# Kernel tuning notes

Measured on AMD Instinct MI355X. Metric: run time of the kernel, lower is better.

The kernel has to match this reference:

```python
import jax, jax.numpy as jnp
import numpy as np

N_HEADS = 4
ITERS = 3
EPS = 1e-8


def layer_norm(x, g, b, eps=1e-5):
    m = jnp.mean(x, axis=-1, keepdims=True)
    v = jnp.mean((x - m) ** 2, axis=-1, keepdims=True)
    return (x - m) * jax.lax.rsqrt(v + eps) * g + b


def gru_cell(x, h, Wih, Whh, bih, bhh):
    # PyTorch GRUCell semantics. x: [M, kvq], h: [M, dim]
    gi = x @ Wih.T + bih
    gh = h @ Whh.T + bhh
    ir, iz, i_n = jnp.split(gi, 3, axis=-1)
    hr, hz, h_n = jnp.split(gh, 3, axis=-1)
    r = jax.nn.sigmoid(ir + hr)
    z = jax.nn.sigmoid(iz + hz)
    n = jnp.tanh(i_n + r * h_n)
    return (1.0 - z) * n + z * h


def slot_attention(features, slots, Wq, Wk, Wv, g_in, b_in, g_s, b_s, Wih, Whh, bih, bhh):
    b, n, _ = features.shape
    _, ns, dim = slots.shape
    kvq = Wk.shape[0]
    dh = kvq // N_HEADS
    scale = dh ** -0.5
    inp = layer_norm(features, g_in, b_in)
    k = (inp @ Wk.T).reshape(b, n, N_HEADS, dh)
    v = (inp @ Wv.T).reshape(b, n, N_HEADS, dh)
    attn_vis = None
    for _ in range(ITERS):
        slots_prev = slots
        s = layer_norm(slots, g_s, b_s)
        q = (s @ Wq.T).reshape(b, ns, N_HEADS, dh)
        dots = jnp.einsum("bihd,bjhd->bihj", q, k) * scale
        attn = jax.nn.softmax(dots, axis=1)  # competitive softmax over slots
        attn_vis = attn.mean(axis=2)  # [b, ns, n]
        w = attn + EPS
        w = w / jnp.sum(w, axis=-1, keepdims=True)  # weighted mean over features
        upd = jnp.einsum("bjhd,bihj->bihd", v, w).reshape(b, ns, kvq)
        slots = gru_cell(upd.reshape(-1, kvq), slots_prev.reshape(-1, dim),
                         Wih, Whh, bih, bhh).reshape(b, ns, dim)
    return slots, attn_vis


def vq_pool(x, codebook):
    # x: [b, ns, d], codebook: [C, d]
    d2 = (jnp.sum(x ** 2, axis=-1, keepdims=True)
          - 2.0 * jnp.einsum("bnd,cd->bnc", x, codebook)
          + jnp.sum(codebook ** 2, axis=-1))
    idx = jnp.argmin(d2, axis=-1)
    q = codebook[idx]
    commit = jnp.mean((x - jax.lax.stop_gradient(q)) ** 2)
    q = x + jax.lax.stop_gradient(q - x)  # straight-through
    return q, idx, commit


def setup_inputs() -> dict:
    key = jax.random.key(0)
    ks = jax.random.split(key, 16)
    B, N, FD = 32, 1024, 768
    NS, D, KVQ, C = 24, 256, 256, 512
    sc = lambda d: d ** -0.5
    return {
        "features": jax.random.normal(ks[0], (B, N, FD), jnp.float32),
        "conditioning": jax.random.normal(ks[1], (B, NS, D), jnp.float32),
        "Wq": jax.random.normal(ks[2], (KVQ, D), jnp.float32) * sc(D),
        "Wk": jax.random.normal(ks[3], (KVQ, FD), jnp.float32) * sc(FD),
        "Wv": jax.random.normal(ks[4], (KVQ, FD), jnp.float32) * sc(FD),
        "g_in": jnp.ones((FD,), jnp.float32),
        "b_in": jnp.zeros((FD,), jnp.float32),
        "g_s": jnp.ones((D,), jnp.float32),
        "b_s": jnp.zeros((D,), jnp.float32),
        "Wih": jax.random.normal(ks[5], (3 * D, KVQ), jnp.float32) * sc(KVQ),
        "Whh": jax.random.normal(ks[6], (3 * D, D), jnp.float32) * sc(D),
        "bih": jnp.zeros((3 * D,), jnp.float32),
        "bhh": jnp.zeros((3 * D,), jnp.float32),
        "codebook": jax.random.normal(ks[7], (C, D), jnp.float32) * sc(D),
    }


def reference(features, conditioning, Wq, Wk, Wv, g_in, b_in, g_s, b_s,
              Wih, Whh, bih, bhh, codebook):
    sa = lambda f, s: slot_attention(f, s, Wq, Wk, Wv, g_in, b_in, g_s, b_s,
                                     Wih, Whh, bih, bhh)
    slots, pre_attn = sa(features, conditioning)
    q_slots, indices, commit = vq_pool(slots, codebook)
    slots, post_attn = sa(features, q_slots)
    return slots, post_attn, pre_attn, indices, commit
```

## Files before the change

### kernel.cpp

```cpp
#include <hip/hip_runtime.h>
#include <math.h>

#define LB __launch_bounds__(256)

constexpr int BATCH = 32, NFEAT = 1024, FDIM = 768, NSLOT = 24;
constexpr int NH = 4, DH = 64, NITER = 3;
constexpr int MF = BATCH * NFEAT;
constexpr int MS = BATCH * NSLOT;
constexpr float QSCALE = 0.125f;
constexpr float ATTN_EPS = 1e-8f;
constexpr float LNEPS = 1e-5f;

typedef __attribute__((ext_vector_type(8))) short bf16x8;
typedef __attribute__((ext_vector_type(4))) float f32x4;

__device__ __forceinline__ unsigned short f2bf(float x) {
  unsigned u = __float_as_uint(x);
  return (unsigned short)((u + 0x7FFFu + ((u >> 16) & 1u)) >> 16);
}
__device__ __forceinline__ float bf2f(unsigned short h) {
  return __uint_as_float(((unsigned)h) << 16);
}
__device__ __forceinline__ void cvt8(const float4& a, const float4& b, float m, float r,
                                     int4& hi, int4& lo) {
  float v[8] = {a.x, a.y, a.z, a.w, b.x, b.y, b.z, b.w};
  unsigned sh[8], sl[8];
#pragma unroll
  for (int j = 0; j < 8; ++j) {
    float vv = (v[j] - m) * r;
    unsigned short h = f2bf(vv);
    sh[j] = h;
    sl[j] = f2bf(vv - bf2f(h));
  }
  hi = make_int4((int)(sh[0] | (sh[1] << 16)), (int)(sh[2] | (sh[3] << 16)),
                 (int)(sh[4] | (sh[5] << 16)), (int)(sh[6] | (sh[7] << 16)));
  lo = make_int4((int)(sl[0] | (sl[1] << 16)), (int)(sl[2] | (sl[3] << 16)),
                 (int)(sl[4] | (sl[5] << 16)), (int)(sl[6] | (sl[7] << 16)));
}

__device__ __forceinline__ void gll16(const void* g, void* l) {
  __builtin_amdgcn_global_load_lds(
      (const __attribute__((address_space(1))) void*)g,
      (__attribute__((address_space(3))) void*)l, 16, 0, 0);
}

__global__ LB void k_preprow(const float* __restrict__ x, float* __restrict__ stats,
                             const float* __restrict__ Wk, const float* __restrict__ Wv,
                             const float* __restrict__ Wq,
                             const float* __restrict__ g_in, const float* __restrict__ b_in,
                             const float* __restrict__ g_s, const float* __restrict__ b_s,
                             short* __restrict__ Bh_g, short* __restrict__ Bl_g,
                             short* __restrict__ Wgqh, short* __restrict__ Wgql,
                             float* __restrict__ cconst) {
  const int t = threadIdx.x;
  if (blockIdx.x < MF / 4) {
    const int row = blockIdx.x * 4 + (t >> 6);
    const int lane = t & 63;
    const float* xr = x + (size_t)row * FDIM;
    float s = 0.f, sq = 0.f;
#pragma unroll
    for (int i = 0; i < 3; ++i) {
      float4 v = *(const float4*)(xr + i * 256 + lane * 4);
      s += v.x + v.y + v.z + v.w;
      sq += v.x * v.x + v.y * v.y + v.z * v.z + v.w * v.w;
    }
#pragma unroll
    for (int o = 32; o > 0; o >>= 1) { s += __shfl_down(s, o, 64); sq += __shfl_down(sq, o, 64); }
    if (lane == 0) {
      float m = s / (float)FDIM;
      float var = sq / (float)FDIM - m * m;
      stats[row * 2] = m;
      stats[row * 2 + 1] = 1.f / sqrtf(var + LNEPS);
    }
    return;
  }
  const int r = blockIdx.x - MF / 4;
  float s = 0.f;
  if (r < 512) {
    const float* srcW = (r < 256) ? (Wk + (size_t)r * FDIM) : (Wv + (size_t)(r - 256) * FDIM);
    for (int k = t; k < FDIM; k += 256) {
      float w = srcW[k];
      float wg = w * g_in[k];
      s += b_in[k] * w;
      unsigned short h = f2bf(wg);
      Bh_g[(size_t)r * FDIM + k] = (short)h;
      Bl_g[(size_t)r * FDIM + k] = (short)f2bf(wg - bf2f(h));
    }
  } else {
    const int c = r - 512;
    float w = Wq[(size_t)c * 256 + t];
    float wg = w * g_s[t];
    unsigned short hh = f2bf(wg);
    Wgqh[(size_t)c * 256 + t] = (short)hh;
    Wgql[(size_t)c * 256 + t] = (short)f2bf(wg - bf2f(hh));
    s = b_s[t] * w;
  }
  __shared__ float red[256];
  red[t] = s; __syncthreads();
  for (int o = 128; o > 0; o >>= 1) { if (t < o) red[t] += red[t + o]; __syncthreads(); }
  if (t == 0) cconst[r] = red[0];
}

union SmemM {
  struct { short Ah[2048], Al[2048], Bh[2][4096], Bl[2][4096]; } m;
  struct { short vh[128][72], vl[128][72]; } e;
};

__global__ LB void k_mfkv(const float* __restrict__ x, const float* __restrict__ stats,
                          const short* __restrict__ Bh_g, const short* __restrict__ Bl_g,
                          const float* __restrict__ cconst,
                          short* __restrict__ khi, short* __restrict__ klo,
                          short* __restrict__ vThi, short* __restrict__ vTlo) {
  __shared__ SmemM sm;
  const int t = threadIdx.x;
  const int l = t & 63;
  const int w = t >> 6;
  const int row0 = blockIdx.x * 64;
  const int c0 = blockIdx.y * 128;

  const int sAr = t >> 2;
  const int sl = t & 3;
  const int kqA = sl ^ ((sAr >> 1) & 3);
  const float* pa = x + (size_t)(row0 + sAr) * FDIM + kqA * 8;
  const float mA = stats[(row0 + sAr) * 2], rA = stats[(row0 + sAr) * 2 + 1];
  const int sBr1 = sAr + 64;
  const int kqB1 = sl ^ ((sBr1 >> 1) & 3);
  const short* pkh0 = Bh_g + (size_t)(c0 + sAr) * FDIM + kqA * 8;
  const short* pkh1 = Bh_g + (size_t)(c0 + sBr1) * FDIM + kqB1 * 8;
  const short* pkl0 = Bl_g + (size_t)(c0 + sAr) * FDIM + kqA * 8;
  const short* pkl1 = Bl_g + (size_t)(c0 + sBr1) * FDIM + kqB1 * 8;
  const short* pvh0 = Bh_g + (size_t)(256 + c0 + sAr) * FDIM + kqA * 8;
  const short* pvh1 = Bh_g + (size_t)(256 + c0 + sBr1) * FDIM + kqB1 * 8;
  const short* pvl0 = Bl_g + (size_t)(256 + c0 + sAr) * FDIM + kqA * 8;
  const short* pvl1 = Bl_g + (size_t)(256 + c0 + sBr1) * FDIM + kqB1 * 8;
  const int wbA = t * 16;
  const int wb0 = t * 16, wb1 = (t + 256) * 16;

  const int wm = (w >> 1) * 32, wn = (w & 1) * 64;
  int aoff[2], boff[4];
#pragma unroll
  for (int m = 0; m < 2; ++m) {
    const int ar = wm + m * 16 + (l & 15);
    const int kq = l >> 4;
    aoff[m] = ar * 64 + ((kq ^ ((ar >> 1) & 3)) << 4);
  }
#pragma unroll
  for (int n = 0; n < 4; ++n) {
    const int bc = wn + n * 16 + (l & 15);
    const int kq = l >> 4;
    boff[n] = bc * 64 + ((kq ^ ((bc >> 1) & 3)) << 4);
  }

  f32x4 acc[2][2][4] = {};
  float4 raa = *(const float4*)pa, rab = *(const float4*)(pa + 4);

  for (int s = 0; s < FDIM / 32; ++s) {
    if (s) __syncthreads();
    const int ko = s * 32;
    gll16(pkh0 + ko, (char*)&sm.m.Bh[0][0] + wb0);
    gll16(pkh1 + ko, (char*)&sm.m.Bh[0][0] + wb1);
    gll16(pkl0 + ko, (char*)&sm.m.Bl[0][0] + wb0);
    gll16(pkl1 + ko, (char*)&sm.m.Bl[0][0] + wb1);
    gll16(pvh0 + ko, (char*)&sm.m.Bh[1][0] + wb0);
    gll16(pvh1 + ko, (char*)&sm.m.Bh[1][0] + wb1);
    gll16(pvl0 + ko, (char*)&sm.m.Bl[1][0] + wb0);
    gll16(pvl1 + ko, (char*)&sm.m.Bl[1][0] + wb1);
    int4 hi, lo;
    cvt8(raa, rab, mA, rA, hi, lo);
    *(int4*)((char*)sm.m.Ah + wbA) = hi; *(int4*)((char*)sm.m.Al + wbA) = lo;
    if (s + 1 < FDIM / 32) {
      raa = *(const float4*)(pa + ko + 32);
      rab = *(const float4*)(pa + ko + 36);
    }
    __syncthreads();
    bf16x8 fah[2], fal[2];
#pragma unroll
    for (int m = 0; m < 2; ++m) {
      fah[m] = *(const bf16x8*)((const char*)sm.m.Ah + aoff[m]);
      fal[m] = *(const bf16x8*)((const char*)sm.m.Al + aoff[m]);
    }
#pragma unroll
    for (int kv = 0; kv < 2; ++kv) {
      bf16x8 fbh[4], fbl[4];
#pragma unroll
      for (int n = 0; n < 4; ++n) {
        fbh[n] = *(const bf16x8*)((const char*)&sm.m.Bh[kv][0] + boff[n]);
        fbl[n] = *(const bf16x8*)((const char*)&sm.m.Bl[kv][0] + boff[n]);
      }
#pragma unroll
      for (int m = 0; m < 2; ++m)
#pragma unroll
        for (int n = 0; n < 4; ++n) {
          acc[kv][m][n] = __builtin_amdgcn_mfma_f32_16x16x32_bf16(fal[m], fbh[n], acc[kv][m][n], 0, 0, 0);
          acc[kv][m][n] = __builtin_amdgcn_mfma_f32_16x16x32_bf16(fah[m], fbl[n], acc[kv][m][n], 0, 0, 0);
          acc[kv][m][n] = __builtin_amdgcn_mfma_f32_16x16x32_bf16(fah[m], fbh[n], acc[kv][m][n], 0, 0, 0);
        }
    }
  }
  __syncthreads();
  const int b_blk = row0 >> 10;
  const int jbase = row0 & 1023;
#pragma unroll
  for (int m = 0; m < 2; ++m) {
    const int rloc = wm + m * 16 + ((l >> 4) << 2);
    const int rbase = row0 + rloc;
#pragma unroll
    for (int n = 0; n < 4; ++n) {
      const int col = wn + n * 16 + (l & 15);
      const int gcol = c0 + col;
      const float cck = cconst[gcol];
      const float ccv = cconst[256 + gcol];
      unsigned vhp[2] = {0, 0}, vlp[2] = {0, 0};
#pragma unroll
      for (int r = 0; r < 4; ++r) {
        const float kval = acc[0][m][n][r] + cck;
        const unsigned short h = f2bf(kval);
        khi[(size_t)(rbase + r) * 256 + gcol] = (short)h;
        klo[(size_t)(rbase + r) * 256 + gcol] = (short)f2bf(kval - bf2f(h));
        const float vval = acc[1][m][n][r] + ccv;
        const unsigned short hv = f2bf(vval);
        const unsigned short lv = f2bf(vval - bf2f(hv));
        vhp[r >> 1] |= ((unsigned)hv) << ((r & 1) * 16);
        vlp[r >> 1] |= ((unsigned)lv) << ((r & 1) * 16);
      }
      *(int2*)((short*)&sm.e.vh[0][0] + col * 72 + rloc) = make_int2((int)vhp[0], (int)vhp[1]);
      *(int2*)((short*)&sm.e.vl[0][0] + col * 72 + rloc) = make_int2((int)vlp[0], (int)vlp[1]);
    }
  }
  __syncthreads();
  {
    const int vr = t >> 1;
    const int vh2 = (t & 1) * 32;
    const int gcol = c0 + vr;
    const int hh2 = gcol >> 6, dh = gcol & 63;
    const size_t vrow = ((size_t)(b_blk * 4 + hh2) * 64 + dh) * 1024 + jbase + vh2;
    const short* sh2 = (const short*)&sm.e.vh[0][0] + vr * 72 + vh2;
    const short* sl2 = (const short*)&sm.e.vl[0][0] + vr * 72 + vh2;
#pragma unroll
    for (int q = 0; q < 4; ++q) {
      *(int4*)(vThi + vrow + q * 8) = *(const int4*)(sh2 + q * 8);
      *(int4*)(vTlo + vrow + q * 8) = *(const int4*)(sl2 + q * 8);
    }
  }
}

template <bool WRITE_ATTN>
__global__ LB void k_fdots(const float* __restrict__ slots,
                           const short* __restrict__ Wgqh, const short* __restrict__ Wgql,
                           const float* __restrict__ cconst,
                           const short* __restrict__ khi, const short* __restrict__ klo,
                           const short* __restrict__ vThi, const short* __restrict__ vTlo,
                           float* __restrict__ attn, float* __restrict__ updp,
                           float* __restrict__ ssump) {
  const int blk = blockIdx.x;
  const int jc = blk & 3;
  const int h = (blk >> 2) & 3;
  const int b = blk >> 4;
  const int t = threadIdx.x;
  const int l = t & 63;
  const int w = t >> 6;
  __shared__ float sc[24 * 256];
  __shared__ short sh_[32 * 256];
  __shared__ short sl_[32 * 256];
  __shared__ short qh[2048], ql[2048];
  __shared__ float part[4][NSLOT];
  __shared__ float mst[NSLOT], rst[NSLOT];

  const short* khb = khi + (size_t)(b * NFEAT + jc * 256) * 256 + h * 64;
  const short* klb = klo + (size_t)(b * NFEAT + jc * 256) * 256 + h * 64;
  bf16x8 kreg[16];
#pragma unroll
  for (int ks = 0; ks < 2; ++ks)
#pragma unroll
    for (int nl = 0; nl < 4; ++nl) {
      const int nt = w * 4 + nl;
      const size_t boffg = (size_t)(nt * 16 + (l & 15)) * 256 + ks * 32 + (l >> 4) * 8;
      kreg[(ks * 4 + nl) * 2 + 0] = *(const bf16x8*)(khb + boffg);
      kreg[(ks * 4 + nl) * 2 + 1] = *(const bf16x8*)(klb + boffg);
    }

  if (t < 192) {
    const int r = t >> 3, g = t & 7;
    const float* sr = slots + (size_t)(b * NSLOT + r) * 256 + g * 32;
    float s = 0.f, sq = 0.f;
#pragma unroll
    for (int m4 = 0; m4 < 8; ++m4) {
      float4 v = *(const float4*)(sr + m4 * 4);
      *(float4*)&sc[r * 256 + g * 32 + m4 * 4] = v;
      s += v.x + v.y + v.z + v.w;
      sq += v.x * v.x + v.y * v.y + v.z * v.z + v.w * v.w;
    }
    s += __shfl_down(s, 4, 8); sq += __shfl_down(sq, 4, 8);
    s += __shfl_down(s, 2, 8); sq += __shfl_down(sq, 2, 8);
    s += __shfl_down(s, 1, 8); sq += __shfl_down(sq, 1, 8);
    if (g == 0) {
      float mm = s * (1.f / 256.f);
      mst[r] = mm;
      rst[r] = 1.f / sqrtf(sq * (1.f / 256.f) - mm * mm + LNEPS);
    }
  }
  __syncthreads();
#pragma unroll 4
  for (int i = 0; i < NSLOT; ++i) {
    const float v = (sc[i * 256 + t] - mst[i]) * rst[i];
    const unsigned short hh = f2bf(v);
    const int slot = i * 32 + ((t >> 3) ^ (i & 31));
    sh_[slot * 8 + (t & 7)] = (short)hh;
    sl_[slot * 8 + (t & 7)] = (short)f2bf(v - bf2f(hh));
  }
  __syncthreads();
  {
    f32x4 qacc[2] = {};
#pragma unroll
    for (int ks = 0; ks < 8; ++ks) {
      bf16x8 ah[2], al[2];
#pragma unroll
      for (int m = 0; m < 2; ++m) {
        const int row = m * 16 + (l & 15);
        const int g = ks * 4 + (l >> 4);
        const int slot = row * 32 + (g ^ (row & 31));
        ah[m] = *(const bf16x8*)&sh_[slot * 8];
        al[m] = *(const bf16x8*)&sl_[slot * 8];
      }
      const size_t brow = (size_t)(h * 64 + w * 16 + (l & 15)) * 256 + ks * 32 + (l >> 4) * 8;
      const bf16x8 bh = *(const bf16x8*)(Wgqh + brow);
      const bf16x8 bl2 = *(const bf16x8*)(Wgql + brow);
#pragma unroll
      for (int m = 0; m < 2; ++m) {
        qacc[m] = __builtin_amdgcn_mfma_f32_16x16x32_bf16(al[m], bh, qacc[m], 0, 0, 0);
        qacc[m] = __builtin_amdgcn_mfma_f32_16x16x32_bf16(ah[m], bl2, qacc[m], 0, 0, 0);
        qacc[m] = __builtin_amdgcn_mfma_f32_16x16x32_bf16(ah[m], bh, qacc[m], 0, 0, 0);
      }
    }
    const int d = w * 16 + (l & 15);
    const float qc = cconst[512 + h * 64 + d];
#pragma unroll
    for (int m = 0; m < 2; ++m)
#pragma unroll
      for (int r = 0; r < 4; ++r) {
        const int row = m * 16 + (l >> 4) * 4 + r;
        const float qv = qacc[m][r] + qc;
        const unsigned short hh = f2bf(qv);
        const int slot = row * 8 + ((d >> 3) ^ (row & 7));
        qh[slot * 8 + (d & 7)] = (short)hh;
        ql[slot * 8 + (d & 7)] = (short)f2bf(qv - bf2f(hh));
      }
  }
  bf16x8 vreg[16];
#pragma unroll
  for (int ks = 0; ks < 8; ++ks) {
    const size_t brow = ((size_t)(b * 4 + h) * 64 + w * 16 + (l & 15)) * 1024 +
                        jc * 256 + ks * 32 + (l >> 4) * 8;
    vreg[ks * 2 + 0] = *(const bf16x8*)(vThi + brow);
    vreg[ks * 2 + 1] = *(const bf16x8*)(vTlo + brow);
  }
  __syncthreads();
  {
    f32x4 scc[2][4] = {};
#pragma unroll
    for (int ks = 0; ks < 2; ++ks) {
      bf16x8 ah[2], al[2];
#pragma unroll
      for (int m = 0; m < 2; ++m) {
        const int row = m * 16 + (l & 15);
        const int g = ks * 4 + (l >> 4);
        const int slot = row * 8 + (g ^ (row & 7));
        ah[m] = *(const bf16x8*)&qh[slot * 8];
        al[m] = *(const bf16x8*)&ql[slot * 8];
      }
#pragma unroll
      for (int nl = 0; nl < 4; ++nl) {
        const bf16x8 bh = kreg[(ks * 4 + nl) * 2 + 0];
        const bf16x8 bl2 = kreg[(ks * 4 + nl) * 2 + 1];
#pragma unroll
        for (int m = 0; m < 2; ++m) {
          scc[m][nl] = __builtin_amdgcn_mfma_f32_16x16x32_bf16(al[m], bh, scc[m][nl], 0, 0, 0);
          scc[m][nl] = __builtin_amdgcn_mfma_f32_16x16x32_bf16(ah[m], bl2, scc[m][nl], 0, 0, 0);
          scc[m][nl] = __builtin_amdgcn_mfma_f32_16x16x32_bf16(ah[m], bh, scc[m][nl], 0, 0, 0);
        }
      }
    }
#pragma unroll
    for (int m = 0; m < 2; ++m)
#pragma unroll
      for (int nl = 0; nl < 4; ++nl) {
        const int col = (w * 4 + nl) * 16 + (l & 15);
        const int rbase = m * 16 + ((l >> 4) << 2);
#pragma unroll
        for (int r = 0; r < 4; ++r)
          if (rbase + r < 24) sc[(rbase + r) * 256 + col] = scc[m][nl][r];
      }
  }
  __syncthreads();
  {
    float acc[NSLOT];
#pragma unroll
    for (int i = 0; i < NSLOT; ++i) acc[i] = sc[i * 256 + t];
    float mx = -1e30f;
#pragma unroll
    for (int i = 0; i < NSLOT; ++i) { acc[i] *= QSCALE; mx = fmaxf(mx, acc[i]); }
    float s = 0.f;
#pragma unroll
    for (int i = 0; i < NSLOT; ++i) { acc[i] = expf(acc[i] - mx); s += acc[i]; }
    const float inv = 1.f / s;
    float* ab = attn + (size_t)(b * NH + h) * NSLOT * NFEAT + jc * 256 + t;
#pragma unroll
    for (int i = 0; i < NSLOT; ++i) {
      const float wgt = acc[i] * inv;
      if (WRITE_ATTN) ab[(size_t)i * NFEAT] = wgt;
      const float ae = wgt + ATTN_EPS;
      acc[i] = ae;
      const unsigned short hh = f2bf(ae);
      const int slot = i * 32 + ((t >> 3) ^ (i & 31));
      sh_[slot * 8 + (t & 7)] = (short)hh;
      sl_[slot * 8 + (t & 7)] = (short)f2bf(ae - bf2f(hh));
    }
#pragma unroll
    for (int i = 0; i < NSLOT; ++i) {
      float rs = acc[i];
#pragma unroll
      for (int o = 32; o > 0; o >>= 1) rs += __shfl_down(rs, o, 64);
      if (l == 0) part[w][i] = rs;
    }
  }
  __syncthreads();
  {
    f32x4 pacc[2] = {};
#pragma unroll
    for (int ks = 0; ks < 8; ++ks) {
      bf16x8 ah[2], al[2];
#pragma unroll
      for (int m = 0; m < 2; ++m) {
        const int row = m * 16 + (l & 15);
        const int g = ks * 4 + (l >> 4);
        const int slot = row * 32 + (g ^ (row & 31));
        ah[m] = *(const bf16x8*)&sh_[slot * 8];
        al[m] = *(const bf16x8*)&sl_[slot * 8];
      }
      const bf16x8 bh = vreg[ks * 2 + 0];
      const bf16x8 bl2 = vreg[ks * 2 + 1];
#pragma unroll
      for (int m = 0; m < 2; ++m) {
        pacc[m] = __builtin_amdgcn_mfma_f32_16x16x32_bf16(al[m], bh, pacc[m], 0, 0, 0);
        pacc[m] = __builtin_amdgcn_mfma_f32_16x16x32_bf16(ah[m], bl2, pacc[m], 0, 0, 0);
        pacc[m] = __builtin_amdgcn_mfma_f32_16x16x32_bf16(ah[m], bh, pacc[m], 0, 0, 0);
      }
    }
    const int d = w * 16 + (l & 15);
    float* up = updp + (size_t)((b * 4 + h) * 4 + jc) * NSLOT * 64;
#pragma unroll
    for (int m = 0; m < 2; ++m)
#pragma unroll
      for (int r = 0; r < 4; ++r) {
        const int row = m * 16 + (l >> 4) * 4 + r;
        if (row < 24) up[row * 64 + d] = pacc[m][r];
      }
  }
  if (t < NSLOT)
    ssump[((size_t)(b * 4 + h) * 4 + jc) * NSLOT + t] =
        part[0][t] + part[1][t] + part[2][t] + part[3][t];
}

template <bool FINAL>
__global__ LB void k_grufin(const float* __restrict__ updp, const float* __restrict__ ssump,
                            const float* __restrict__ sprev,
                            const float* __restrict__ Wih, const float* __restrict__ Whh,
                            const float* __restrict__ bih, const float* __restrict__ bhh,
                            float* __restrict__ snext, float* __restrict__ outs,
                            const float* __restrict__ attn, float* __restrict__ vis_out) {
  __shared__ float updt[8][256];
  __shared__ float Bs[3][64][33];
  const int bx = blockIdx.x;
  const int d0 = blockIdx.y * 32;
  const int rows0 = bx * 8;
  const int t = threadIdx.x;
  {
    const int h = t >> 6, d = t & 63;
#pragma unroll
    for (int u = 0; u < 8; ++u) {
      const int row = rows0 + u;
      const int b = row / 24, i = row - b * 24;
      const size_t base = (size_t)(b * 4 + h) * 4;
      float s = 0.f, wsum = 0.f;
#pragma unroll
      for (int jc = 0; jc < 4; ++jc) {
        s += updp[(base + jc) * (NSLOT * 64) + i * 64 + d];
        wsum += ssump[(base + jc) * NSLOT + i];
      }
      updt[u][h * 64 + d] = s / wsum;
    }
  }
  __syncthreads();
  const int r = t >> 5;
  const int dd = t & 31;
  float accR = 0.f, accZ = 0.f, accN = 0.f, accH = 0.f;
  for (int k0 = 0; k0 < 256; k0 += 64) {
#pragma unroll
    for (int ii = 0; ii < 6; ++ii) {
      const int i = ii * 256 + t;
      const int s = i / 512, rem = i & 511, c = rem >> 4, kq = rem & 15;
      float4 wv = *(const float4*)(Wih + (size_t)(s * 256 + d0 + c) * 256 + k0 + kq * 4);
      Bs[s][kq * 4 + 0][c] = wv.x; Bs[s][kq * 4 + 1][c] = wv.y;
      Bs[s][kq * 4 + 2][c] = wv.z; Bs[s][kq * 4 + 3][c] = wv.w;
    }
    __syncthreads();
#pragma unroll
    for (int kk = 0; kk < 64; ++kk) {
      const float a = updt[r][k0 + kk];
      accR += a * Bs[0][kk][dd];
      accZ += a * Bs[1][kk][dd];
      accN += a * Bs[2][kk][dd];
    }
    __syncthreads();
  }
  {
    const int rr2 = t >> 5, c0 = (t & 31) * 8;
    const float* sp = sprev + (size_t)(rows0 + rr2) * 256 + c0;
    *(float4*)&updt[rr2][c0] = *(const float4*)sp;
    *(float4*)&updt[rr2][c0 + 4] = *(const float4*)(sp + 4);
  }
  __syncthreads();
  for (int k0 = 0; k0 < 256; k0 += 64) {
#pragma unroll
    for (int ii = 0; ii < 6; ++ii) {
      const int i = ii * 256 + t;
      const int s = i / 512, rem = i & 511, c = rem >> 4, kq = rem & 15;
      float4 wv = *(const float4*)(Whh + (size_t)(s * 256 + d0 + c) * 256 + k0 + kq * 4);
      Bs[s][kq * 4 + 0][c] = wv.x; Bs[s][kq * 4 + 1][c] = wv.y;
      Bs[s][kq * 4 + 2][c] = wv.z; Bs[s][kq * 4 + 3][c] = wv.w;
    }
    __syncthreads();
#pragma unroll
    for (int kk = 0; kk < 64; ++kk) {
      const float a = updt[r][k0 + kk];
      accR += a * Bs[0][kk][dd];
      accZ += a * Bs[1][kk][dd];
      accH += a * Bs[2][kk][dd];
    }
    __syncthreads();
  }
  const int row = rows0 + r;
  const int c = d0 + dd;
  const float hp = updt[r][c];
  const float rr = 1.f / (1.f + expf(-(accR + bih[c] + bhh[c])));
  const float zz = 1.f / (1.f + expf(-(accZ + bih[256 + c] + bhh[256 + c])));
  const float nn = tanhf(accN + bih[512 + c] + rr * (accH + bhh[512 + c]));
  const float o = (1.f - zz) * nn + zz * hp;
  snext[(size_t)row * 256 + c] = o;
  if (FINAL) {
    outs[(size_t)row * 256 + c] = o;
    const int gid = (blockIdx.y * 96 + blockIdx.x) * 256 + t;
#pragma unroll
    for (int z = 0; z < 4; ++z) {
      const int idx = z * 196608 + gid;
      const int j = idx & 1023;
      const int rem = idx >> 10;
      const int i = rem % NSLOT;
      const int b = rem / NSLOT;
      float s = 0.f;
#pragma unroll
      for (int hh = 0; hh < NH; ++hh)
        s += attn[(size_t)((b * NH + hh) * NSLOT + i) * NFEAT + j];
      vis_out[idx] = 0.25f * s;
    }
  }
}

__global__ LB void k_vqvis(float* __restrict__ slots, const float* __restrict__ cb,
                           const float* __restrict__ attn,
                           float* __restrict__ idx_out, float* __restrict__ bestd2,
                           float* __restrict__ vis_out) {
  const int t = threadIdx.x;
  if (blockIdx.x >= MS) {
    const int idx = (blockIdx.x - MS) * 256 + t;
    const int j = idx & 1023;
    const int rem = idx >> 10;
    const int i = rem % NSLOT;
    const int b = rem / NSLOT;
    float s = 0.f;
#pragma unroll
    for (int h = 0; h < NH; ++h)
      s += attn[(size_t)((b * NH + h) * NSLOT + i) * NFEAT + j];
    vis_out[idx] = 0.25f * s;
    return;
  }
  const int r = blockIdx.x;
  __shared__ float xs[256];
  __shared__ float red[256];
  __shared__ float rv[256];
  __shared__ int ri[256];
  xs[t] = slots[(size_t)r * 256 + t];
  __syncthreads();
  red[t] = xs[t] * xs[t]; __syncthreads();
  for (int o = 128; o > 0; o >>= 1) { if (t < o) red[t] += red[t + o]; __syncthreads(); }
  const float x2 = red[0];
  float best = 1e30f; int bidx = 0;
#pragma unroll
  for (int cset = 0; cset < 2; ++cset) {
    const int c = cset * 256 + t;
    const float* cr = cb + (size_t)c * 256;
    float xc = 0.f, cc = 0.f;
    for (int dd = 0; dd < 256; dd += 4) {
      float4 cv = *(const float4*)(cr + dd);
      xc += xs[dd] * cv.x + xs[dd + 1] * cv.y + xs[dd + 2] * cv.z + xs[dd + 3] * cv.w;
      cc += cv.x * cv.x + cv.y * cv.y + cv.z * cv.z + cv.w * cv.w;
    }
    float d2 = x2 - 2.f * xc + cc;
    if (d2 < best) { best = d2; bidx = c; }
  }
  rv[t] = best; ri[t] = bidx; __syncthreads();
  for (int o = 128; o > 0; o >>= 1) {
    if (t < o) {
      if (rv[t + o] < rv[t] || (rv[t + o] == rv[t] && ri[t + o] < ri[t])) {
        rv[t] = rv[t + o]; ri[t] = ri[t + o];
      }
    }
    __syncthreads();
  }
  const int wi = ri[0];
  const float cval = cb[(size_t)wi * 256 + t];
  const float diff = xs[t] - cval;
  red[t] = diff * diff; __syncthreads();
  for (int o = 128; o > 0; o >>= 1) { if (t < o) red[t] += red[t + o]; __syncthreads(); }
  if (t == 0) { idx_out[r] = (float)wi; bestd2[r] = red[0]; }
  slots[(size_t)r * 256 + t] = cval;
}

__global__ LB void k_commit(const float* __restrict__ bestd2, float* __restrict__ out) {
  const int t = threadIdx.x;
  __shared__ float red[256];
  float s = 0.f;
  for (int i = t; i < MS; i += 256) s += bestd2[i];
  red[t] = s; __syncthreads();
  for (int o = 128; o > 0; o >>= 1) { if (t < o) red[t] += red[t + o]; __syncthreads(); }
  if (t == 0) out[0] = red[0] / (float)(MS * 256);
}

extern "C" void kernel_launch(void* const* d_in, const int* in_sizes, int n_in,
                              void* d_out, int out_size, void* d_ws, size_t ws_size,
                              hipStream_t stream) {
  const float* features = (const float*)d_in[0];
  const float* cond = (const float*)d_in[1];
  const float* Wq = (const float*)d_in[2];
  const float* Wk = (const float*)d_in[3];
  const float* Wv = (const float*)d_in[4];
  const float* g_in = (const float*)d_in[5];
  const float* b_in = (const float*)d_in[6];
  const float* g_s = (const float*)d_in[7];
  const float* b_s = (const float*)d_in[8];
  const float* Wih = (const float*)d_in[9];
  const float* Whh = (const float*)d_in[10];
  const float* bih = (const float*)d_in[11];
  const float* bhh = (const float*)d_in[12];
  const float* cb = (const float*)d_in[13];
  float* out = (float*)d_out;

  char* wsb = (char*)d_ws;
  short* Bh_g = (short*)wsb; wsb += (size_t)512 * FDIM * 2;
  short* Bl_g = (short*)wsb; wsb += (size_t)512 * FDIM * 2;
  short* khi = (short*)wsb; wsb += (size_t)MF * 256 * 2;
  short* klo = (short*)wsb; wsb += (size_t)MF * 256 * 2;
  short* vThi = (short*)wsb; wsb += (size_t)MF * 256 * 2;
  short* vTlo = (short*)wsb; wsb += (size_t)MF * 256 * 2;
  short* Wgqh = (short*)wsb; wsb += (size_t)256 * 256 * 2;
  short* Wgql = (short*)wsb; wsb += (size_t)256 * 256 * 2;
  float* ws = (float*)wsb;
  float* stats = ws;  ws += 2 * MF;
  float* attn = ws;   ws += (size_t)BATCH * NH * NSLOT * NFEAT;
  float* sbufA = ws;  ws += (size_t)MS * 256;
  float* sbufB = ws;  ws += (size_t)MS * 256;
  float* updp = ws;   ws += (size_t)512 * NSLOT * 64;
  float* ssump = ws;  ws += (size_t)512 * NSLOT;
  float* cconst = ws; ws += 768;
  float* bestd2 = ws; ws += MS;

  float* out_slots = out;
  float* out_post = out + 196608;
  float* out_pre = out + 196608 + 786432;
  float* out_idx = out + 196608 + 786432 * 2;
  float* out_commit = out_idx + 768;

  k_preprow<<<MF / 4 + 768, 256, 0, stream>>>(features, stats, Wk, Wv, Wq, g_in, b_in,
                                              g_s, b_s, Bh_g, Bl_g, Wgqh, Wgql, cconst);
  k_mfkv<<<dim3(MF / 64, 2), 256, 0, stream>>>(features, stats, Bh_g, Bl_g, cconst,
                                               khi, klo, vThi, vTlo);

  const float* scur = cond;
  float* bufs[2] = {sbufA, sbufB};
  int nb = 0;
  for (int call = 0; call < 2; ++call) {
    for (int it = 0; it < NITER; ++it) {
      float* snxt = bufs[nb]; nb ^= 1;
      if (it == NITER - 1)
        k_fdots<true><<<512, 256, 0, stream>>>(scur, Wgqh, Wgql, cconst, khi, klo,
                                               vThi, vTlo, attn, updp, ssump);
      else
        k_fdots<false><<<512, 256, 0, stream>>>(scur, Wgqh, Wgql, cconst, khi, klo,
                                                vThi, vTlo, attn, updp, ssump);
      if (call == 1 && it == NITER - 1)
        k_grufin<true><<<dim3(MS / 8, 8), 256, 0, stream>>>(updp, ssump, scur, Wih, Whh,
                                                            bih, bhh, snxt, out_slots,
                                                            attn, out_post);
      else
        k_grufin<false><<<dim3(MS / 8, 8), 256, 0, stream>>>(updp, ssump, scur, Wih, Whh,
                                                             bih, bhh, snxt, out_slots,
                                                             nullptr, nullptr);
      scur = snxt;
    }
    if (call == 0) {
      k_vqvis<<<MS + BATCH * NSLOT * NFEAT / 256, 256, 0, stream>>>(
          (float*)scur, cb, attn, out_idx, bestd2, out_pre);
      k_commit<<<1, 256, 0, stream>>>(bestd2, out_commit);
    }
  }
}
```

Measured before the change: 546.2 us.

## Alias LDS buffers in fdots kernel and fuse slot LayerNorm into registers

Merges the fp32 score buffer and the bf16 hi/lo staging buffers into one shared 32 KB arena, shrinking the block's LDS footprint to raise occupancy. The slot LayerNorm now keeps the loaded values in registers and writes normalized bf16 hi/lo pairs straight from them using wave shuffles, which drops one barrier and the fp32 staging round-trip. The V register prefetch is moved after the score MFMAs, which shortens register live ranges but exposes more of the V load latency before the PV product. An extra barrier is added so the aliased arena is fully read before it is overwritten.

```diff
diff --git a/kernel.cpp b/kernel.cpp
--- a/kernel.cpp
+++ b/kernel.cpp
@@ -259,12 +259,12 @@
   const int t = threadIdx.x;
   const int l = t & 63;
   const int w = t >> 6;
-  __shared__ float sc[24 * 256];
-  __shared__ short sh_[32 * 256];
-  __shared__ short sl_[32 * 256];
+  __shared__ __attribute__((aligned(16))) char arena[32768];
+  short* snh = (short*)arena;
+  short* snl = (short*)(arena + 16384);
+  float* scF = (float*)arena;
   __shared__ short qh[2048], ql[2048];
   __shared__ float part[4][NSLOT];
-  __shared__ float mst[NSLOT], rst[NSLOT];
 
   const short* khb = khi + (size_t)(b * NFEAT + jc * 256) * 256 + h * 64;
   const short* klb = klo + (size_t)(b * NFEAT + jc * 256) * 256 + h * 64;
@@ -282,31 +282,31 @@
   if (t < 192) {
     const int r = t >> 3, g = t & 7;
     const float* sr = slots + (size_t)(b * NSLOT + r) * 256 + g * 32;
+    float4 va[8];
     float s = 0.f, sq = 0.f;
 #pragma unroll
     for (int m4 = 0; m4 < 8; ++m4) {
-      float4 v = *(const float4*)(sr + m4 * 4);
-      *(float4*)&sc[r * 256 + g * 32 + m4 * 4] = v;
-      s += v.x + v.y + v.z + v.w;
-      sq += v.x * v.x + v.y * v.y + v.z * v.z + v.w * v.w;
+      va[m4] = *(const float4*)(sr + m4 * 4);
+      s += va[m4].x + va[m4].y + va[m4].z + va[m4].w;
+      sq += va[m4].x * va[m4].x + va[m4].y * va[m4].y +
+            va[m4].z * va[m4].z + va[m4].w * va[m4].w;
     }
     s += __shfl_down(s, 4, 8); sq += __shfl_down(sq, 4, 8);
     s += __shfl_down(s, 2, 8); sq += __shfl_down(sq, 2, 8);
     s += __shfl_down(s, 1, 8); sq += __shfl_down(sq, 1, 8);
-    if (g == 0) {
-      float mm = s * (1.f / 256.f);
-      mst[r] = mm;
-      rst[r] = 1.f / sqrtf(sq * (1.f / 256.f) - mm * mm + LNEPS);
-    }
-  }
-  __syncthreads();
-#pragma unroll 4
-  for (int i = 0; i < NSLOT; ++i) {
-    const float v = (sc[i * 256 + t] - mst[i]) * rst[i];
-    const unsigned short hh = f2bf(v);
-    const int slot = i * 32 + ((t >> 3) ^ (i & 31));
-    sh_[slot * 8 + (t & 7)] = (short)hh;
-    sl_[slot * 8 + (t & 7)] = (short)f2bf(v - bf2f(hh));
+    const float st = __shfl(s, l & 56, 64);
+    const float sqt = __shfl(sq, l & 56, 64);
+    const float mm = st * (1.f / 256.f);
+    const float rr = 1.f / sqrtf(sqt * (1.f / 256.f) - mm * mm + LNEPS);
+#pragma unroll
+    for (int m4 = 0; m4 < 8; m4 += 2) {
+      int4 hi, lo;
+      cvt8(va[m4], va[m4 + 1], mm, rr, hi, lo);
+      const int gi = g * 4 + (m4 >> 1);
+      const int slot = r * 32 + (gi ^ (r & 31));
+      *(int4*)&snh[slot * 8] = hi;
+      *(int4*)&snl[slot * 8] = lo;
+    }
   }
   __syncthreads();
   {
@@ -319,8 +319,8 @@
         const int row = m * 16 + (l & 15);
         const int g = ks * 4 + (l >> 4);
         const int slot = row * 32 + (g ^ (row & 31));
-        ah[m] = *(const bf16x8*)&sh_[slot * 8];
-        al[m] = *(const bf16x8*)&sl_[slot * 8];
+        ah[m] = *(const bf16x8*)&snh[slot * 8];
+        al[m] = *(const bf16x8*)&snl[slot * 8];
       }
       const size_t brow = (size_t)(h * 64 + w * 16 + (l & 15)) * 256 + ks * 32 + (l >> 4) * 8;
       const bf16x8 bh = *(const bf16x8*)(Wgqh + brow);
@@ -346,14 +346,6 @@
         ql[slot * 8 + (d & 7)] = (short)f2bf(qv - bf2f(hh));
       }
   }
-  bf16x8 vreg[16];
-#pragma unroll
-  for (int ks = 0; ks < 8; ++ks) {
-    const size_t brow = ((size_t)(b * 4 + h) * 64 + w * 16 + (l & 15)) * 1024 +
-                        jc * 256 + ks * 32 + (l >> 4) * 8;
-    vreg[ks * 2 + 0] = *(const bf16x8*)(vThi + brow);
-    vreg[ks * 2 + 1] = *(const bf16x8*)(vTlo + brow);
-  }
   __syncthreads();
   {
     f32x4 scc[2][4] = {};
@@ -388,14 +380,23 @@
         const int rbase = m * 16 + ((l >> 4) << 2);
 #pragma unroll
         for (int r = 0; r < 4; ++r)
-          if (rbase + r < 24) sc[(rbase + r) * 256 + col] = scc[m][nl][r];
-      }
-  }
+          if (rbase + r < 24) scF[(rbase + r) * 256 + col] = scc[m][nl][r];
+      }
+  }
+  bf16x8 vreg[16];
+#pragma unroll
+  for (int ks = 0; ks < 8; ++ks) {
+    const size_t brow = ((size_t)(b * 4 + h) * 64 + w * 16 + (l & 15)) * 1024 +
+                        jc * 256 + ks * 32 + (l >> 4) * 8;
+    vreg[ks * 2 + 0] = *(const bf16x8*)(vThi + brow);
+    vreg[ks * 2 + 1] = *(const bf16x8*)(vTlo + brow);
+  }
+  __syncthreads();
+  float acc[NSLOT];
+#pragma unroll
+  for (int i = 0; i < NSLOT; ++i) acc[i] = scF[i * 256 + t];
   __syncthreads();
   {
-    float acc[NSLOT];
-#pragma unroll
-    for (int i = 0; i < NSLOT; ++i) acc[i] = sc[i * 256 + t];
     float mx = -1e30f;
 #pragma unroll
     for (int i = 0; i < NSLOT; ++i) { acc[i] *= QSCALE; mx = fmaxf(mx, acc[i]); }
@@ -412,8 +413,8 @@
       acc[i] = ae;
       const unsigned short hh = f2bf(ae);
       const int slot = i * 32 + ((t >> 3) ^ (i & 31));
-      sh_[slot * 8 + (t & 7)] = (short)hh;
-      sl_[slot * 8 + (t & 7)] = (short)f2bf(ae - bf2f(hh));
+      snh[slot * 8 + (t & 7)] = (short)hh;
+      snl[slot * 8 + (t & 7)] = (short)f2bf(ae - bf2f(hh));
     }
 #pragma unroll
     for (int i = 0; i < NSLOT; ++i) {
@@ -434,8 +435,8 @@
         const int row = m * 16 + (l & 15);
         const int g = ks * 4 + (l >> 4);
         const int slot = row * 32 + (g ^ (row & 31));
-        ah[m] = *(const bf16x8*)&sh_[slot * 8];
-        al[m] = *(const bf16x8*)&sl_[slot * 8];
+        ah[m] = *(const bf16x8*)&snh[slot * 8];
+        al[m] = *(const bf16x8*)&snl[slot * 8];
       }
       const bf16x8 bh = vreg[ks * 2 + 0];
       const bf16x8 bl2 = vreg[ks * 2 + 1];
```

After: 544.2 us. No clear change (-0.4%).
